# Performance work log

Measured on AMD Instinct MI355X. Metric: run time of the kernel, lower is better.

The kernel has to match this reference:

```python
import jax, jax.numpy as jnp
import numpy as np

ALPHA = 0.2  # LeakyReLU negative slope
NEG_INF = -1.0e12


def setup_inputs() -> dict:
    key = jax.random.key(0)
    k1, k2, k3, k4 = jax.random.split(key, 4)
    B, N, Fin, Fout = 4, 4096, 256, 128
    inp = jax.random.normal(k1, (B, N, Fin), dtype=jnp.float32)
    adj_weights = jax.random.uniform(k2, (B, N, N), dtype=jnp.float32)
    W = jax.random.normal(k3, (Fin, Fout), dtype=jnp.float32) * (1.414 / np.sqrt(Fin))
    a = jax.random.normal(k4, (2 * Fout, 1), dtype=jnp.float32) * 0.1
    return {"inp": inp, "adj_weights": adj_weights, "W": W, "a": a}


def reference(inp, adj_weights, W, a):
    Fout = W.shape[1]
    h = jnp.matmul(inp, W)                       # [B, N, Fout]
    # a_input[b,i,j] = concat(h[b,i], h[b,j]); matmul with a splits into two rank-1 terms
    a1 = a[:Fout, 0]                             # [Fout]
    a2 = a[Fout:, 0]                             # [Fout]
    s1 = jnp.einsum('bnf,f->bn', h, a1)          # [B, N]
    s2 = jnp.einsum('bnf,f->bn', h, a2)          # [B, N]
    e = jax.nn.leaky_relu(s1[:, :, None] + s2[:, None, :], negative_slope=ALPHA)  # [B,N,N]
    attention = jnp.where(adj_weights > 0, adj_weights * e, NEG_INF)
    attention = jax.nn.softmax(attention, axis=2)
    # dropout p=0.0 / eval mode -> identity
    h_prime = jnp.matmul(attention, h)           # [B, N, Fout]
    return jax.nn.elu(h_prime)                   # concat=True branch
```

## Files before the change

kernel.cpp:

```cpp
#include <hip/hip_runtime.h>
#include <math.h>

typedef float    float4_t __attribute__((ext_vector_type(4)));
typedef _Float16 half8    __attribute__((ext_vector_type(8)));

#define NEG_BIG (-1.0e12f)

__global__ __launch_bounds__(256) void k_prep(const float* __restrict__ inp,
                                              const float* __restrict__ W,
                                              const float* __restrict__ a,
                                              float* __restrict__ s1,
                                              float* __restrict__ s2,
                                              _Float16* __restrict__ hT) {
    __shared__ float sA[32 * 68];
    __shared__ float sW[64 * 128];
    const int t   = threadIdx.x;
    const int gr0 = blockIdx.x * 32;
    const int b   = gr0 >> 12;
    const int f0  = (t & 15) * 8;
    const int r0  = (t >> 4) * 2;
    float4_t acc0[2] = {}; float4_t acc1[2] = {};
    for (int kc = 0; kc < 4; ++kc) {
        __syncthreads();
        #pragma unroll
        for (int it = 0; it < 2; ++it) {
            int fi = it * 256 + t; int r = fi >> 4; int c = (fi & 15) * 4;
            *(float4_t*)&sA[r * 68 + c] =
                *(const float4_t*)&inp[(size_t)(gr0 + r) * 256 + kc * 64 + c];
        }
        #pragma unroll
        for (int it = 0; it < 8; ++it) {
            int fi = it * 256 + t; int k = fi >> 5; int c = (fi & 31) * 4;
            *(float4_t*)&sW[k * 128 + c] =
                *(const float4_t*)&W[(size_t)(kc * 64 + k) * 128 + c];
        }
        __syncthreads();
        for (int k = 0; k < 64; ++k) {
            float4_t w0 = *(const float4_t*)&sW[k * 128 + f0];
            float4_t w1 = *(const float4_t*)&sW[k * 128 + f0 + 4];
            #pragma unroll
            for (int r = 0; r < 2; ++r) {
                float av = sA[(r0 + r) * 68 + k];
                acc0[r] += av * w0; acc1[r] += av * w1;
            }
        }
    }
    float4_t a1lo = *(const float4_t*)&a[f0];
    float4_t a1hi = *(const float4_t*)&a[f0 + 4];
    float4_t a2lo = *(const float4_t*)&a[128 + f0];
    float4_t a2hi = *(const float4_t*)&a[128 + f0 + 4];
    #pragma unroll
    for (int r = 0; r < 2; ++r) {
        const int row  = gr0 + r0 + r;
        const int rloc = row & 4095;
        #pragma unroll
        for (int c = 0; c < 4; ++c) {
            hT[(size_t)b * (128 * 4096) + (size_t)(f0 + c) * 4096 + rloc]     = (_Float16)acc0[r][c];
            hT[(size_t)b * (128 * 4096) + (size_t)(f0 + 4 + c) * 4096 + rloc] = (_Float16)acc1[r][c];
        }
        float p1 = acc0[r][0]*a1lo[0] + acc0[r][1]*a1lo[1] + acc0[r][2]*a1lo[2] + acc0[r][3]*a1lo[3]
                 + acc1[r][0]*a1hi[0] + acc1[r][1]*a1hi[1] + acc1[r][2]*a1hi[2] + acc1[r][3]*a1hi[3];
        float p2 = acc0[r][0]*a2lo[0] + acc0[r][1]*a2lo[1] + acc0[r][2]*a2lo[2] + acc0[r][3]*a2lo[3]
                 + acc1[r][0]*a2hi[0] + acc1[r][1]*a2hi[1] + acc1[r][2]*a2hi[2] + acc1[r][3]*a2hi[3];
        #pragma unroll
        for (int o = 1; o < 16; o <<= 1) { p1 += __shfl_xor(p1, o); p2 += __shfl_xor(p2, o); }
        if ((t & 15) == 0) { s1[row] = p1; s2[row] = p2; }
    }
}

__global__ __launch_bounds__(256) void k_s2max(const float* __restrict__ s2,
                                               float* __restrict__ s2max) {
    const int b = blockIdx.x, t = threadIdx.x;
    float m = -INFINITY;
    for (int i = t; i < 4096; i += 256) m = fmaxf(m, s2[b * 4096 + i]);
    #pragma unroll
    for (int o = 1; o < 64; o <<= 1) m = fmaxf(m, __shfl_xor(m, o));
    __shared__ float sm[4];
    if ((t & 63) == 0) sm[t >> 6] = m;
    __syncthreads();
    if (t == 0) s2max[b] = fmaxf(fmaxf(sm[0], sm[1]), fmaxf(sm[2], sm[3]));
}

__global__ __launch_bounds__(256, 4) void k_flash(const float* __restrict__ adj,
                                                  const _Float16* __restrict__ hT,
                                                  const float* __restrict__ s1,
                                                  const float* __restrict__ s2,
                                                  const float* __restrict__ s2max,
                                                  float* __restrict__ part_acc,
                                                  float* __restrict__ part_l) {
    const int t    = threadIdx.x;
    const int bid  = blockIdx.x;
    const int sp   = bid & 3;
    const int rb   = (bid >> 2) & 63;
    const int b    = bid >> 8;
    const int w    = t >> 6, lane = t & 63;
    const int quad = lane >> 4, ln15 = lane & 15;
    const int rowb  = rb * 64 + w * 16;
    const int myrow = rowb + ln15;
    const float*    adj_r = adj + (size_t)b * 4096 * 4096 + (size_t)myrow * 4096;
    const _Float16* hT_b  = hT + (size_t)b * 128 * 4096;
    const float*    s2_b  = s2 + b * 4096;
    const float s1v  = s1[b * 4096 + myrow];
    const float mhat = fmaxf(0.f, s1v + s2max[b]);
    const int jwbase = sp * 1024;
    const int coff   = quad * 8;

    float4_t acc[8] = {};
    float psum = 0.f;

    float4_t adjc[4], adjn[4];
    #pragma unroll
    for (int kc = 0; kc < 2; ++kc) {
        adjc[kc * 2 + 0] = *(const float4_t*)&adj_r[jwbase + kc * 32 + coff];
        adjc[kc * 2 + 1] = *(const float4_t*)&adj_r[jwbase + kc * 32 + coff + 4];
    }
    for (int jt = 0; jt < 16; ++jt) {
        const int j0 = jwbase + jt * 64;
        if (jt < 15) {
            #pragma unroll
            for (int kc = 0; kc < 2; ++kc) {
                adjn[kc * 2 + 0] = *(const float4_t*)&adj_r[j0 + 64 + kc * 32 + coff];
                adjn[kc * 2 + 1] = *(const float4_t*)&adj_r[j0 + 64 + kc * 32 + coff + 4];
            }
        }
        float4_t s2v[4];
        #pragma unroll
        for (int kc = 0; kc < 2; ++kc) {
            s2v[kc * 2 + 0] = *(const float4_t*)&s2_b[j0 + kc * 32 + coff];
            s2v[kc * 2 + 1] = *(const float4_t*)&s2_b[j0 + kc * 32 + coff + 4];
        }
        half8 afrag[2];
        #pragma unroll
        for (int kc = 0; kc < 2; ++kc) {
            #pragma unroll
            for (int hh = 0; hh < 2; ++hh) {
                float4_t av = adjc[kc * 2 + hh];
                float4_t sv = s2v[kc * 2 + hh];
                #pragma unroll
                for (int c = 0; c < 4; ++c) {
                    float x   = s1v + sv[c];
                    float e   = x > 0.f ? x : 0.2f * x;
                    float p   = av[c] > 0.f ? __expf(av[c] * e - mhat) : 0.f;
                    _Float16 q = (_Float16)p;
                    afrag[kc][hh * 4 + c] = q;
                    psum += (float)q;
                }
            }
        }
        #pragma unroll
        for (int nt = 0; nt < 8; ++nt) {
            #pragma unroll
            for (int kc = 0; kc < 2; ++kc) {
                half8 bfrag = *(const half8*)&hT_b[(size_t)(nt * 16 + ln15) * 4096 + j0 + kc * 32 + coff];
                acc[nt] = __builtin_amdgcn_mfma_f32_16x16x32_f16(afrag[kc], bfrag, acc[nt], 0, 0, 0);
            }
        }
        #pragma unroll
        for (int q2 = 0; q2 < 4; ++q2) adjc[q2] = adjn[q2];
    }
    psum += __shfl_xor(psum, 16);
    psum += __shfl_xor(psum, 32);
    const size_t growb = (size_t)b * 4096 + rowb;
    if (lane < 16) part_l[(size_t)sp * 16384 + growb + lane] = psum;
    float* pacc = part_acc + (size_t)sp * 16384 * 128;
    #pragma unroll
    for (int nt = 0; nt < 8; ++nt) {
        #pragma unroll
        for (int reg = 0; reg < 4; ++reg) {
            pacc[(growb + quad * 4 + reg) * 128 + nt * 16 + ln15] = acc[nt][reg];
        }
    }
}

__global__ __launch_bounds__(256) void k_combine(const float* __restrict__ part_acc,
                                                 const float* __restrict__ part_l,
                                                 float* __restrict__ out) {
    const int idx = blockIdx.x * 256 + threadIdx.x;
    const int e0  = idx * 4;
    const int gr  = e0 >> 7;
    float l = part_l[gr] + part_l[16384 + gr] + part_l[32768 + gr] + part_l[49152 + gr];
    float4_t a0 = *(const float4_t*)&part_acc[e0];
    float4_t a1 = *(const float4_t*)&part_acc[2097152 + e0];
    float4_t a2 = *(const float4_t*)&part_acc[4194304 + e0];
    float4_t a3 = *(const float4_t*)&part_acc[6291456 + e0];
    float4_t s  = (a0 + a1) + (a2 + a3);
    float rl = 1.f / l;
    float4_t o;
    #pragma unroll
    for (int c = 0; c < 4; ++c) {
        float v = s[c] * rl;
        o[c] = v > 0.f ? v : expm1f(v);
    }
    *(float4_t*)&((float*)out)[e0] = o;
}

extern "C" void kernel_launch(void* const* d_in, const int* in_sizes, int n_in,
                              void* d_out, int out_size, void* d_ws, size_t ws_size,
                              hipStream_t stream) {
    const float* inp = (const float*)d_in[0];
    const float* adj = (const float*)d_in[1];
    const float* W   = (const float*)d_in[2];
    const float* a   = (const float*)d_in[3];
    float* out = (float*)d_out;

    char* wsb = (char*)d_ws;
    _Float16* hT       = (_Float16*)(wsb);
    float*    s1       = (float*)(wsb + 4194304);
    float*    s2       = (float*)(wsb + 4259840);
    float*    s2max    = (float*)(wsb + 4325376);
    float*    part_l   = (float*)(wsb + 4325632);
    float*    part_acc = (float*)(wsb + 4587776);

    hipLaunchKernelGGL(k_prep,    dim3(512),  dim3(256), 0, stream, inp, W, a, s1, s2, hT);
    hipLaunchKernelGGL(k_s2max,   dim3(4),    dim3(256), 0, stream, s2, s2max);
    hipLaunchKernelGGL(k_flash,   dim3(1024), dim3(256), 0, stream, adj, hT, s1, s2, s2max,
                       part_acc, part_l);
    hipLaunchKernelGGL(k_combine, dim3(2048), dim3(256), 0, stream, part_acc, part_l, out);
}
```

Before: 514.8 us.

## Stage hT tiles in double-buffered swizzled LDS shared across waves in k_flash

Each 64-column tile of hT is now loaded cooperatively by the block into a double-buffered, XOR-swizzled shared memory buffer, and the MFMA B fragments are read from LDS instead of directly from global memory. Before this, each of the four waves separately fetched the same hT data from global or L2. The next tile is prefetched into registers while the current one is computed, at the cost of a __syncthreads per tile and 32KB of LDS per block, which may lower occupancy.

```diff
diff --git a/kernel.cpp b/kernel.cpp
--- a/kernel.cpp
+++ b/kernel.cpp
@@ -3,8 +3,6 @@
 
 typedef float    float4_t __attribute__((ext_vector_type(4)));
 typedef _Float16 half8    __attribute__((ext_vector_type(8)));
-
-#define NEG_BIG (-1.0e12f)
 
 __global__ __launch_bounds__(256) void k_prep(const float* __restrict__ inp,
                                               const float* __restrict__ W,
@@ -88,6 +86,8 @@
                                                   const float* __restrict__ s2max,
                                                   float* __restrict__ part_acc,
                                                   float* __restrict__ part_l) {
+    __shared__ _Float16 hbuf[2][128 * 64];
+
     const int t    = threadIdx.x;
     const int bid  = blockIdx.x;
     const int sp   = bid & 3;
@@ -105,6 +105,10 @@
     const int jwbase = sp * 1024;
     const int coff   = quad * 8;
 
+    const int sf  = t >> 3;
+    const int sc  = t & 7;
+    const int fb7 = ln15 & 7;
+
     float4_t acc[8] = {};
     float psum = 0.f;
 
@@ -114,33 +118,49 @@
         adjc[kc * 2 + 0] = *(const float4_t*)&adj_r[jwbase + kc * 32 + coff];
         adjc[kc * 2 + 1] = *(const float4_t*)&adj_r[jwbase + kc * 32 + coff + 4];
     }
+    {
+        half8 hreg[4];
+        #pragma unroll
+        for (int i = 0; i < 4; ++i) {
+            int f = i * 32 + sf;
+            hreg[i] = *(const half8*)&hT_b[(size_t)f * 4096 + jwbase + sc * 8];
+        }
+        #pragma unroll
+        for (int i = 0; i < 4; ++i) {
+            int f = i * 32 + sf;
+            *(half8*)&hbuf[0][f * 64 + ((sc ^ (f & 7)) << 3)] = hreg[i];
+        }
+    }
+    __syncthreads();
+
     for (int jt = 0; jt < 16; ++jt) {
-        const int j0 = jwbase + jt * 64;
+        const int cur = jt & 1;
+        const int j0  = jwbase + jt * 64;
+        half8 hreg[4];
         if (jt < 15) {
+            #pragma unroll
+            for (int i = 0; i < 4; ++i) {
+                int f = i * 32 + sf;
+                hreg[i] = *(const half8*)&hT_b[(size_t)f * 4096 + j0 + 64 + sc * 8];
+            }
             #pragma unroll
             for (int kc = 0; kc < 2; ++kc) {
                 adjn[kc * 2 + 0] = *(const float4_t*)&adj_r[j0 + 64 + kc * 32 + coff];
                 adjn[kc * 2 + 1] = *(const float4_t*)&adj_r[j0 + 64 + kc * 32 + coff + 4];
             }
         }
-        float4_t s2v[4];
+        half8 afrag[2];
         #pragma unroll
         for (int kc = 0; kc < 2; ++kc) {
-            s2v[kc * 2 + 0] = *(const float4_t*)&s2_b[j0 + kc * 32 + coff];
-            s2v[kc * 2 + 1] = *(const float4_t*)&s2_b[j0 + kc * 32 + coff + 4];
-        }
-        half8 afrag[2];
-        #pragma unroll
-        for (int kc = 0; kc < 2; ++kc) {
             #pragma unroll
             for (int hh = 0; hh < 2; ++hh) {
+                float4_t sv = *(const float4_t*)&s2_b[j0 + kc * 32 + coff + hh * 4];
                 float4_t av = adjc[kc * 2 + hh];
-                float4_t sv = s2v[kc * 2 + hh];
                 #pragma unroll
                 for (int c = 0; c < 4; ++c) {
-                    float x   = s1v + sv[c];
-                    float e   = x > 0.f ? x : 0.2f * x;
-                    float p   = av[c] > 0.f ? __expf(av[c] * e - mhat) : 0.f;
+                    float x = s1v + sv[c];
+                    float e = x > 0.f ? x : 0.2f * x;
+                    float p = av[c] > 0.f ? __expf(av[c] * e - mhat) : 0.f;
                     _Float16 q = (_Float16)p;
                     afrag[kc][hh * 4 + c] = q;
                     psum += (float)q;
@@ -151,12 +171,21 @@
         for (int nt = 0; nt < 8; ++nt) {
             #pragma unroll
             for (int kc = 0; kc < 2; ++kc) {
-                half8 bfrag = *(const half8*)&hT_b[(size_t)(nt * 16 + ln15) * 4096 + j0 + kc * 32 + coff];
+                const int fb = nt * 16 + ln15;
+                half8 bfrag = *(const half8*)&hbuf[cur][fb * 64 + ((((kc << 2) + quad) ^ fb7) << 3)];
                 acc[nt] = __builtin_amdgcn_mfma_f32_16x16x32_f16(afrag[kc], bfrag, acc[nt], 0, 0, 0);
             }
         }
-        #pragma unroll
-        for (int q2 = 0; q2 < 4; ++q2) adjc[q2] = adjn[q2];
+        if (jt < 15) {
+            #pragma unroll
+            for (int i = 0; i < 4; ++i) {
+                int f = i * 32 + sf;
+                *(half8*)&hbuf[1 - cur][f * 64 + ((sc ^ (f & 7)) << 3)] = hreg[i];
+            }
+            #pragma unroll
+            for (int q2 = 0; q2 < 4; ++q2) adjc[q2] = adjn[q2];
+        }
+        __syncthreads();
     }
     psum += __shfl_xor(psum, 16);
     psum += __shfl_xor(psum, 32);
```

Result: faster. 442.2 us (-14.1%).
